# Performance work log

Hardware: AMD Instinct MI355X
Metric: run time of the kernel (lower is better)

The kernel has to match this reference:

```python
import jax, jax.numpy as jnp
import numpy as np

B, TK, NK, H, E, V = 128, 400, 50, 256, 256, 50000


def setup_inputs() -> dict:
    key = jax.random.key(0)
    ks = iter(jax.random.split(key, 48))
    def rn(shape, s=1.0):
        return jax.random.normal(next(ks), shape, jnp.float32) * s
    def ru(shape):
        return jax.random.uniform(next(ks), shape, jnp.float32)
    z = lambda shape: jnp.zeros(shape, jnp.float32)
    s = 0.05
    inp = {}
    inp['y_t_1'] = jax.random.randint(next(ks), (B,), 0, V)
    inp['h_prev'] = rn((B, H))
    inp['c_prev'] = rn((B, H))
    inp['encoder_outputs'] = rn((B, TK, H))
    inp['encoder_outputs_node'] = rn((B, NK, H))
    inp['enc_padding_mask'] = jnp.ones((B, TK), jnp.float32)
    inp['enc_padding_mask_node'] = jnp.ones((B, NK), jnp.float32)
    inp['c_t_d'] = rn((B, H))
    inp['c_t_g'] = rn((B, H))
    inp['c_t_g2'] = rn((B, H))
    inp['coverage'] = z((B, TK))
    inp['flow'] = ru((B, NK))
    inp['node_to_token'] = ru((B, NK, TK))
    inp['graph'] = ru((B, NK, NK))
    inp['voc_d'] = jax.random.randint(next(ks), (B, TK), 0, V)
    inp['step'] = 0
    # learned parameters
    inp['emb_table'] = rn((V, E), s)
    inp['Wx'] = rn((4 * H, E), s); inp['bx'] = z((E,))
    inp['Wi'] = rn((E, 4 * H), s); inp['Wh'] = rn((H, 4 * H), s)
    inp['bi'] = z((4 * H,)); inp['bh'] = z((4 * H,))
    inp['Whd'] = rn((H, H), s); inp['Wsd'] = rn((2 * H, H), s)
    inp['wcd'] = rn((H,), s); inp['vd'] = rn((H,), s); inp['bd'] = z((H,))
    inp['Wn'] = rn((H, H), s); inp['Wsf'] = rn((2 * H, H), s)
    inp['vf'] = rn((H,), s); inp['bf'] = z((H,))
    inp['Wpg'] = rn((5 * H + E, 1), s); inp['bpg'] = z((1,))
    inp['W1'] = rn((4 * H, H), s); inp['b1'] = z((H,))
    inp['W2'] = rn((H, V), s); inp['b2'] = z((V,))
    return inp


def _forward(y_t_1, h_prev, c_prev, enc, enc_n, mask_t, mask_n, c_t_d, c_t_g, c_t_g2,
             coverage, flow, n2t, graph, voc_d, emb_table, Wx, bx, Wi, Wh, bi, bh,
             Whd, Wsd, wcd, vd, bd, Wn, Wsf, vf, bf, Wpg, bpg, W1, b1, W2, b2):
    sig, tanh = jax.nn.sigmoid, jnp.tanh
    y_emb = emb_table[y_t_1]                                   # [B,E]
    x = jnp.concatenate([c_t_d, c_t_g, c_t_g2, y_emb], 1) @ Wx + bx
    # single-step LSTM (torch gate order i,f,g,o)
    gates = x @ Wi + h_prev @ Wh + bi + bh
    gi, gf, gg, go = jnp.split(gates, 4, axis=1)
    c_new = sig(gf) * c_prev + sig(gi) * tanh(gg)
    h_new = sig(go) * tanh(c_new)
    s_hat = jnp.concatenate([h_new, c_new], 1)                 # [B,2H]
    # doc attention with coverage (Bahdanau)
    e = tanh(enc @ Whd + (s_hat @ Wsd)[:, None, :] + coverage[:, :, None] * wcd + bd) @ vd
    a = jax.nn.softmax(e, axis=1) * mask_t
    a = a / a.sum(1, keepdims=True)                            # [B,TK]
    c_d = jnp.einsum('bt,bth->bh', a, enc)
    coverage_next = coverage + a
    # event-graph node attention (flow-weighted, one-hop propagation)
    en = tanh(enc_n @ Wn + (s_hat @ Wsf)[:, None, :] + bf) @ vf
    an = jax.nn.softmax(en, axis=1) * mask_n
    an = an / an.sum(1, keepdims=True)
    an = an * flow
    an = an / an.sum(1, keepdims=True)                         # [B,NK]
    c_g = jnp.einsum('bn,bnh->bh', an, enc_n)
    an2 = jnp.einsum('bn,bnm->bm', an, graph) * mask_n
    an2 = an2 / an2.sum(1, keepdims=True)
    c_g2 = jnp.einsum('bn,bnh->bh', an2, enc_n)
    a_n2t = jnp.einsum('bn,bnt->bt', an, n2t)
    a_n2t = a_n2t / a_n2t.sum(1, keepdims=True)
    # flow update: per-node max of token attention restricted to node tokens
    flow_ = jnp.max(a[:, None, :] * n2t, axis=2)               # [B,NK]
    flow_next = flow_ / flow_.sum(1, keepdims=True)
    # pointer-generator gate
    p_gen = sig(jnp.concatenate([c_d, c_g, c_g2, s_hat, x], 1) @ Wpg + bpg)  # [B,1]
    out = jnp.concatenate([h_new, c_d, c_g, c_g2], 1) @ W1 + b1
    vocab_dist = jax.nn.softmax(out @ W2 + b2, axis=1)         # [B,V]
    attn_all = a / a.sum(1, keepdims=True)
    attn_ = (1.0 - p_gen) * attn_all
    vocab_ = p_gen * vocab_dist
    rows = jnp.arange(vocab_.shape[0])[:, None]
    final_dist = vocab_.at[rows, voc_d].add(attn_)             # scatter_add over vocab
    return (final_dist, (h_new, c_new), c_d, c_g, c_g2, a, a_n2t, p_gen,
            coverage_next, flow_next)


def reference(y_t_1, h_prev, c_prev, encoder_outputs, encoder_outputs_node,
              enc_padding_mask, enc_padding_mask_node, c_t_d, c_t_g, c_t_g2,
              coverage, flow, node_to_token, graph, voc_d, step,
              emb_table, Wx, bx, Wi, Wh, bi, bh, Whd, Wsd, wcd, vd, bd,
              Wn, Wsf, vf, bf, Wpg, bpg, W1, b1, W2, b2):
    return _forward(y_t_1, h_prev, c_prev, encoder_outputs, encoder_outputs_node,
                    enc_padding_mask, enc_padding_mask_node, c_t_d, c_t_g, c_t_g2,
                    coverage, flow, node_to_token, graph, voc_d, emb_table, Wx, bx,
                    Wi, Wh, bi, bh, Whd, Wsd, wcd, vd, bd, Wn, Wsf, vf, bf,
                    Wpg, bpg, W1, b1, W2, b2)
```

## Files before the change

kernel.cpp:

```cpp
#include <hip/hip_runtime.h>
#include <stdint.h>


typedef unsigned short u16;
typedef unsigned int   u32;

#define Bv  128
#define TKv 400
#define NKv 50
#define Hv  256
#define Vv  50000
#define VPAD 50176
#define NSv 16
#define CHUNKv 3136
#define MDOC (Bv * TKv)
#define MNODE (Bv * NKv)
#define NBLK (VPAD / 64)

typedef __attribute__((ext_vector_type(8))) short bf16x8;
typedef __attribute__((ext_vector_type(4))) float f32x4;

__device__ float g_x[32768];
__device__ float g_xp[4 * 32768];
__device__ float g_gates[131072];
__device__ float g_h[32768];
__device__ float g_c[32768];
__device__ float g_sdp[2 * 32768];
__device__ float g_sfp[2 * 32768];
__device__ float g_ep[4 * MDOC];
__device__ float g_enp[4 * MNODE];
__device__ float g_a[51200];
__device__ float g_cd[32768];
__device__ float g_cdp[8 * 32768];
__device__ float g_cg[32768];
__device__ float g_cg2[32768];
__device__ float g_pg[128];
__device__ float g_ans[MNODE];
__device__ float g_inv4[128];
__device__ float g_fl[MNODE];
__device__ float g_nrs[MNODE];
__device__ float g_o1[32768];
__device__ __attribute__((aligned(16))) u16 g_o1b[32768];
__device__ float g_vpp[(size_t)2 * Bv * NBLK];
__device__ float g_vred[Bv * 2];
__device__ float g_logits[6400000];
__device__ u16   g_Wdt[256 * 256];
__device__ u16   g_Wnt[256 * 256];
__device__ u16   g_W2t[(size_t)VPAD * 256];
__device__ u16   g_encb[(size_t)Bv * TKv * 256];
__device__ u16   g_encnb[(size_t)Bv * NKv * 256];

__device__ __forceinline__ float sigm(float x) { return 1.f / (1.f + expf(-x)); }

__device__ __forceinline__ u16 f2bf(float f) {
    u32 u = __float_as_uint(f);
    return (u16)((u + 0x7fffu + ((u >> 16) & 1u)) >> 16);
}

__device__ __forceinline__ bf16x8 cvt8(const float* __restrict__ p) {
    const float4 a = *(const float4*)p;
    const float4 b = *(const float4*)(p + 4);
    bf16x8 r;
    r[0] = (short)f2bf(a.x); r[1] = (short)f2bf(a.y);
    r[2] = (short)f2bf(a.z); r[3] = (short)f2bf(a.w);
    r[4] = (short)f2bf(b.x); r[5] = (short)f2bf(b.y);
    r[6] = (short)f2bf(b.z); r[7] = (short)f2bf(b.w);
    return r;
}

__device__ __forceinline__ float fast_tanh(float x) {
    x = fminf(fmaxf(x, -15.f), 15.f);
    float e = __expf(2.f * x);
    return (e - 1.f) / (e + 1.f);
}

__device__ __forceinline__ void ms_merge(float& m1, float& s1, float m2, float s2) {
    float M = fmaxf(m1, m2);
    s1 = s1 * expf(m1 - M) + s2 * expf(m2 - M);
    m1 = M;
}

__global__ __launch_bounds__(256) void k_cvt(
    const float* __restrict__ src, u16* __restrict__ dst, int n8)
{
    int i = blockIdx.x * 256 + threadIdx.x;
    const int stride = gridDim.x * 256;
    for (; i < n8; i += stride)
        *(bf16x8*)(dst + (size_t)i * 8) = cvt8(src + (size_t)i * 8);
}

__global__ __launch_bounds__(256) void k_tc(
    const float* __restrict__ src, u16* __restrict__ dst, int K, int N)
{
    __shared__ float tile[32][33];
    const int n0 = blockIdx.x * 32, k0 = blockIdx.y * 32;
    const int tx = threadIdx.x & 31, ty = threadIdx.x >> 5;
    #pragma unroll
    for (int i = 0; i < 32; i += 8) {
        int k = k0 + ty + i, n = n0 + tx;
        tile[ty + i][tx] = (n < N) ? src[(size_t)k * N + n] : 0.f;
    }
    __syncthreads();
    #pragma unroll
    for (int i = 0; i < 32; i += 8) {
        int n = n0 + ty + i, k = k0 + tx;
        dst[(size_t)n * K + k] = f2bf(tile[tx][ty + i]);
    }
}

__global__ __launch_bounds__(256) void k_x(
    const int* __restrict__ y,
    const float* __restrict__ ctd, const float* __restrict__ ctg,
    const float* __restrict__ ctg2, const float* __restrict__ emb,
    const float* __restrict__ Wx)
{
    const int b = blockIdx.x, ks = blockIdx.y, j = threadIdx.x;
    __shared__ float cs[256];
    float v;
    if      (ks == 0) v = ctd [b * 256 + j];
    else if (ks == 1) v = ctg [b * 256 + j];
    else if (ks == 2) v = ctg2[b * 256 + j];
    else              v = emb[(size_t)y[b] * 256 + j];
    cs[j] = v;
    __syncthreads();

    float acc = 0.f;
    const float* w = Wx + (size_t)(ks * 256) * 256 + j;
    #pragma unroll 8
    for (int k = 0; k < 256; k++) acc += cs[k] * w[(size_t)k * 256];
    g_xp[ks * 32768 + b * 256 + j] = acc;
}

__global__ __launch_bounds__(256) void k_gates(
    const float* __restrict__ h_prev,
    const float* __restrict__ Wi, const float* __restrict__ Wh,
    const float* __restrict__ bi, const float* __restrict__ bh,
    const float* __restrict__ bx)
{
    const int b = blockIdx.x, cc = blockIdx.y, j = threadIdx.x;
    __shared__ float xs[256], hs[256];

    float xv = bx[j] + g_xp[b * 256 + j] + g_xp[32768 + b * 256 + j]
             + g_xp[65536 + b * 256 + j] + g_xp[98304 + b * 256 + j];
    xs[j] = xv;
    if (cc == 0) g_x[b * 256 + j] = xv;
    hs[j] = h_prev[b * 256 + j];
    __syncthreads();

    const int col = cc * 256 + j;
    float acc = bi[col] + bh[col];
    const float* wi = Wi + col;
    const float* wh = Wh + col;
    #pragma unroll 8
    for (int k = 0; k < 256; k++)
        acc += xs[k] * wi[(size_t)k * 1024] + hs[k] * wh[(size_t)k * 1024];
    g_gates[b * 1024 + col] = acc;
}

__global__ __launch_bounds__(256) void k_cellsd(
    const float* __restrict__ c_prev,
    const float* __restrict__ Wsd, const float* __restrict__ Wsf,
    float* __restrict__ out_h, float* __restrict__ out_c)
{
    const int b = blockIdx.x, ks = blockIdx.y, j = threadIdx.x;
    __shared__ float sh[256];

    const float* gb = g_gates + b * 1024;
    float gi_ = gb[j], gf_ = gb[256 + j], gg_ = gb[512 + j], go_ = gb[768 + j];
    float cp = c_prev[b * 256 + j];
    float cn = sigm(gf_) * cp + sigm(gi_) * tanhf(gg_);
    float hn = sigm(go_) * tanhf(cn);
    if (ks == 0) {
        g_h[b * 256 + j] = hn;  g_c[b * 256 + j] = cn;
        out_h[b * 256 + j] = hn; out_c[b * 256 + j] = cn;
    }
    sh[j] = (ks == 0) ? hn : cn;
    __syncthreads();

    float asd = 0.f, asf = 0.f;
    const float* wd = Wsd + (size_t)(ks * 256) * 256 + j;
    const float* wf = Wsf + (size_t)(ks * 256) * 256 + j;
    #pragma unroll 8
    for (int k = 0; k < 256; k++) {
        float sv = sh[k];
        asd += sv * wd[(size_t)k * 256];
        asf += sv * wf[(size_t)k * 256];
    }
    g_sdp[ks * 32768 + b * 256 + j] = asd;
    g_sfp[ks * 32768 + b * 256 + j] = asf;
}

template<int R>
__global__ __launch_bounds__(256) void k_scores(
    const u16* __restrict__ srcb,
    const u16* __restrict__ Wt,
    const float* __restrict__ addv0,
    const float* __restrict__ addv1,
    const float* __restrict__ abias,
    const float* __restrict__ cov,
    const float* __restrict__ wcw,
    const float* __restrict__ vv,
    float* __restrict__ eout, int Mtot)
{
    const int tid = threadIdx.x;
    const int lane = tid & 63, w = tid >> 6;
    const int nlow = lane & 15, quad = lane >> 4;
    const int c0 = blockIdx.y * 64;

    __shared__ u16 Bs[64][264];
    {
        const u16* wsrc = Wt + (size_t)c0 * 256;
        #pragma unroll
        for (int j = 0; j < 8; j++) {
            int chunk = tid + j * 256;
            int row = chunk >> 5, c16 = chunk & 31;
            *(bf16x8*)(&Bs[row][c16 * 8]) =
                *(const bf16x8*)(wsrc + row * 256 + c16 * 8);
        }
    }
    __syncthreads();

    const int rowbase = blockIdx.x * 128 + w * 32;
    const u16* a0 = srcb + (size_t)(rowbase + nlow) * 256 + quad * 8;
    const u16* a1 = a0 + 16 * 256;

    const f32x4 zf = {0.f, 0.f, 0.f, 0.f};
    f32x4 acc[2][4];
    #pragma unroll
    for (int mi = 0; mi < 2; mi++)
        #pragma unroll
        for (int ni = 0; ni < 4; ni++) acc[mi][ni] = zf;

    bf16x8 af0 = *(const bf16x8*)(a0);
    bf16x8 af1 = *(const bf16x8*)(a1);
    for (int k0 = 0; k0 < 256; k0 += 32) {
        const int kn = (k0 + 32) & 255;
        bf16x8 nf0 = *(const bf16x8*)(a0 + kn);
        bf16x8 nf1 = *(const bf16x8*)(a1 + kn);
        bf16x8 bf[4];
        #pragma unroll
        for (int ni = 0; ni < 4; ni++)
            bf[ni] = *(const bf16x8*)(&Bs[ni * 16 + nlow][k0 + quad * 8]);
        #pragma unroll
        for (int ni = 0; ni < 4; ni++) {
            acc[0][ni] = __builtin_amdgcn_mfma_f32_16x16x32_bf16(af0, bf[ni], acc[0][ni], 0, 0, 0);
            acc[1][ni] = __builtin_amdgcn_mfma_f32_16x16x32_bf16(af1, bf[ni], acc[1][ni], 0, 0, 0);
        }
        af0 = nf0; af1 = nf1;
    }

    #pragma unroll
    for (int mi = 0; mi < 2; mi++) {
        float covt[4]; int bidx[4];
        #pragma unroll
        for (int r = 0; r < 4; r++) {
            int row = rowbase + mi * 16 + quad * 4 + r;
            covt[r] = cov ? cov[row] : 0.f;
            bidx[r] = row / R;
        }
        float s4[4] = {0.f, 0.f, 0.f, 0.f};
        #pragma unroll
        for (int ni = 0; ni < 4; ni++) {
            int col = c0 + ni * 16 + nlow;
            float vvc = vv[col];
            float ab  = abias[col];
            float wcc = wcw ? wcw[col] : 0.f;
            #pragma unroll
            for (int r = 0; r < 4; r++) {
                float adc = addv0[bidx[r] * 256 + col] + addv1[bidx[r] * 256 + col] + ab;
                s4[r] += vvc * fast_tanh(acc[mi][ni][r] + adc + covt[r] * wcc);
            }
        }
        #pragma unroll
        for (int r = 0; r < 4; r++) {
            float s = s4[r];
            s += __shfl_xor(s, 1, 64);
            s += __shfl_xor(s, 2, 64);
            s += __shfl_xor(s, 4, 64);
            s += __shfl_xor(s, 8, 64);
            int row = rowbase + mi * 16 + quad * 4 + r;
            if (nlow == 0)
                eout[(size_t)blockIdx.y * Mtot + row] = s;
        }
    }
}

__global__ __launch_bounds__(256) void k_doc(
    const float* __restrict__ mask,
    const float* __restrict__ cov,
    float* __restrict__ out_a, float* __restrict__ out_cov)
{
    const int b = blockIdx.x, tid = threadIdx.x;
    __shared__ float red[256];

    float e0 = 0.f, e1s = 0.f;
    #pragma unroll
    for (int ch = 0; ch < 4; ch++) {
        e0 += g_ep[ch * MDOC + b * TKv + tid];
        if (tid + 256 < TKv) e1s += g_ep[ch * MDOC + b * TKv + tid + 256];
    }
    float e1 = (tid + 256 < TKv) ? e1s : -1e30f;

    float m = fmaxf(e0, e1);
    red[tid] = m; __syncthreads();
    for (int s = 128; s > 0; s >>= 1) { if (tid < s) red[tid] = fmaxf(red[tid], red[tid + s]); __syncthreads(); }
    m = red[0]; __syncthreads();

    float p0 = expf(e0 - m) * mask[b * TKv + tid];
    float p1 = (tid + 256 < TKv) ? expf(e1 - m) * mask[b * TKv + tid + 256] : 0.f;
    red[tid] = p0 + p1; __syncthreads();
    for (int s = 128; s > 0; s >>= 1) { if (tid < s) red[tid] += red[tid + s]; __syncthreads(); }
    float inv = 1.f / red[0];

    float a0 = p0 * inv;
    g_a[b * TKv + tid] = a0;
    out_a[b * TKv + tid] = a0;
    out_cov[b * TKv + tid] = cov[b * TKv + tid] + a0;
    if (tid + 256 < TKv) {
        float a1 = p1 * inv;
        g_a[b * TKv + tid + 256] = a1;
        out_a[b * TKv + tid + 256] = a1;
        out_cov[b * TKv + tid + 256] = cov[b * TKv + tid + 256] + a1;
    }
}

__global__ __launch_bounds__(256) void k_cd(const float* __restrict__ enc)
{
    const int b = blockIdx.x, ks = blockIdx.y, tid = threadIdx.x;
    __shared__ float as_[50];
    if (tid < 50) as_[tid] = g_a[b * TKv + ks * 50 + tid];
    __syncthreads();

    const float* eb = enc + ((size_t)b * TKv + ks * 50) * 256 + tid;
    float acc = 0.f;
    #pragma unroll 10
    for (int t = 0; t < 50; t++) acc += as_[t] * eb[(size_t)t * 256];
    g_cdp[ks * 32768 + b * 256 + tid] = acc;
}

__global__ __launch_bounds__(256) void k_fmax(const float* __restrict__ n2t)
{
    const int bn = blockIdx.x;
    const int b = bn / NKv;
    const int tid = threadIdx.x;
    __shared__ float rmx[256], rsm[256];

    const float* nb = n2t + (size_t)bn * TKv;
    const float* ab = g_a + b * TKv;

    float x0 = nb[tid], a0 = ab[tid];
    float mx = a0 * x0, sm = x0;
    if (tid + 256 < TKv) {
        float x1 = nb[tid + 256], a1 = ab[tid + 256];
        mx = fmaxf(mx, a1 * x1);
        sm += x1;
    }
    mx = fmaxf(mx, 0.f);
    rmx[tid] = mx; rsm[tid] = sm; __syncthreads();
    for (int s = 128; s > 0; s >>= 1) {
        if (tid < s) {
            rmx[tid] = fmaxf(rmx[tid], rmx[tid + s]);
            rsm[tid] += rsm[tid + s];
        }
        __syncthreads();
    }
    if (tid == 0) { g_fl[bn] = rmx[0]; g_nrs[bn] = rsm[0]; }
}

__global__ __launch_bounds__(64) void k_flow2(float* __restrict__ out_flow)
{
    const int b = blockIdx.x, tid = threadIdx.x;
    float v = (tid < NKv) ? g_fl[b * NKv + tid] : 0.f;
    float s = v;
    s += __shfl_xor(s, 1, 64);
    s += __shfl_xor(s, 2, 64);
    s += __shfl_xor(s, 4, 64);
    s += __shfl_xor(s, 8, 64);
    s += __shfl_xor(s, 16, 64);
    s += __shfl_xor(s, 32, 64);
    if (tid < NKv) out_flow[b * NKv + tid] = v / s;
}

__global__ __launch_bounds__(256) void k_node1(
    const float* __restrict__ encn,
    const float* __restrict__ maskn,
    const float* __restrict__ flow,
    const float* __restrict__ graph,
    const float* __restrict__ Wpg, const float* __restrict__ bpg,
    float* __restrict__ out_cd, float* __restrict__ out_cg,
    float* __restrict__ out_cg2, float* __restrict__ out_pgen)
{
    const int b = blockIdx.x, tid = threadIdx.x;
    __shared__ float ans[NKv], an2s[NKv], red[256];

    float cd = 0.f;
    #pragma unroll
    for (int i = 0; i < 8; i++) cd += g_cdp[i * 32768 + b * 256 + tid];
    g_cd[b * 256 + tid] = cd;
    out_cd[b * 256 + tid] = cd;

    float v = -1e30f;
    if (tid < NKv) {
        v = 0.f;
        #pragma unroll
        for (int ch = 0; ch < 4; ch++) v += g_enp[ch * MNODE + b * NKv + tid];
    }
    red[tid] = v; __syncthreads();
    for (int s = 128; s > 0; s >>= 1) { if (tid < s) red[tid] = fmaxf(red[tid], red[tid + s]); __syncthreads(); }
    float m = red[0]; __syncthreads();

    float p = (tid < NKv) ? expf(v - m) * maskn[b * NKv + tid] : 0.f;
    red[tid] = p; __syncthreads();
    for (int s = 128; s > 0; s >>= 1) { if (tid < s) red[tid] += red[tid + s]; __syncthreads(); }
    float S = red[0]; __syncthreads();
    p = (tid < NKv) ? (p / S) * flow[b * NKv + tid] : 0.f;
    red[tid] = p; __syncthreads();
    for (int s = 128; s > 0; s >>= 1) { if (tid < s) red[tid] += red[tid + s]; __syncthreads(); }
    float S2 = red[0]; __syncthreads();
    if (tid < NKv) {
        ans[tid] = p / S2;
        g_ans[b * NKv + tid] = ans[tid];
    }
    __syncthreads();

    float s4p = (tid < NKv) ? ans[tid] * g_nrs[b * NKv + tid] : 0.f;
    red[tid] = s4p; __syncthreads();
    for (int s = 128; s > 0; s >>= 1) { if (tid < s) red[tid] += red[tid + s]; __syncthreads(); }
    if (tid == 0) g_inv4[b] = 1.f / red[0];
    __syncthreads();

    float q = 0.f;
    if (tid < NKv) {
        const float* gb = graph + (size_t)b * NKv * NKv + tid;
        #pragma unroll
        for (int n = 0; n < NKv; n++) q += ans[n] * gb[n * NKv];
        q *= maskn[b * NKv + tid];
    }
    red[tid] = q; __syncthreads();
    for (int s = 128; s > 0; s >>= 1) { if (tid < s) red[tid] += red[tid + s]; __syncthreads(); }
    float S3 = red[0]; __syncthreads();
    if (tid < NKv) an2s[tid] = q / S3;
    __syncthreads();

    float cg = 0.f, cg2 = 0.f;
    {
        const float* enb = encn + (size_t)b * NKv * 256 + tid;
        #pragma unroll
        for (int n = 0; n < NKv; n++) {
            float e = enb[n * 256];
            cg  += ans[n]  * e;
            cg2 += an2s[n] * e;
        }
    }
    g_cg[b * 256 + tid] = cg;   out_cg[b * 256 + tid] = cg;
    g_cg2[b * 256 + tid] = cg2; out_cg2[b * 256 + tid] = cg2;

    float hvv = g_h[b * 256 + tid], cvv = g_c[b * 256 + tid];
    float xvv = g_x[b * 256 + tid];
    float part = cd  * Wpg[tid]        + cg  * Wpg[256 + tid]
               + cg2 * Wpg[512 + tid]  + hvv * Wpg[768 + tid]
               + cvv * Wpg[1024 + tid] + xvv * Wpg[1280 + tid];
    red[tid] = part; __syncthreads();
    for (int s = 128; s > 0; s >>= 1) { if (tid < s) red[tid] += red[tid + s]; __syncthreads(); }
    if (tid == 0) {
        float pg = sigm(red[0] + bpg[0]);
        g_pg[b] = pg; out_pgen[b] = pg;
    }
}

__global__ __launch_bounds__(256) void k_ant(
    const float* __restrict__ n2t, float* __restrict__ out_ant)
{
    const int b = blockIdx.x, ks = blockIdx.y, tid = threadIdx.x;
    __shared__ float ans[NKv];
    if (tid < NKv) ans[tid] = g_ans[b * NKv + tid];
    __syncthreads();

    if (tid < 200) {
        const int t = ks * 200 + tid;
        const float* nb = n2t + (size_t)b * NKv * TKv + t;
        float at = 0.f;
        #pragma unroll
        for (int n = 0; n < NKv; n++) at += ans[n] * nb[n * TKv];
        out_ant[b * TKv + t] = at * g_inv4[b];
    }
}

__global__ __launch_bounds__(256) void k_o1(
    const float* __restrict__ W1, const float* __restrict__ b1)
{
    const int b = blockIdx.x, cc = blockIdx.y, tid = threadIdx.x;
    __shared__ float cat[1024];
    __shared__ float red[256];

    cat[tid]       = g_h  [b * 256 + tid];
    cat[256 + tid] = g_cd [b * 256 + tid];
    cat[512 + tid] = g_cg [b * 256 + tid];
    cat[768 + tid] = g_cg2[b * 256 + tid];
    __syncthreads();

    const int lane = tid & 63, kq = tid >> 6;
    const int col = cc * 64 + lane;
    const float* w  = W1 + (size_t)(kq * 256) * 256 + col;
    const float* cs = cat + kq * 256;
    float acc = 0.f;
    #pragma unroll 8
    for (int k = 0; k < 256; k++) acc += cs[k] * w[(size_t)k * 256];
    red[tid] = acc; __syncthreads();

    if (tid < 64) {
        float o = b1[cc * 64 + tid]
                + red[tid] + red[64 + tid] + red[128 + tid] + red[192 + tid];
        g_o1[b * 256 + cc * 64 + tid] = o;
        g_o1b[b * 256 + cc * 64 + tid] = f2bf(o);
    }
}

__global__ __launch_bounds__(256) void k_logits(const float* __restrict__ b2)
{
    const int v0 = blockIdx.x * 64;
    const int tid = threadIdx.x;
    const int lane = tid & 63, wave = tid >> 6;
    const int nlow = lane & 15, quad = lane >> 4;

    const u16* a0p = g_o1b + (wave * 32 + nlow) * 256 + quad * 8;
    const u16* a1p = a0p + 16 * 256;
    const u16* bbase = g_W2t + (size_t)(v0 + nlow) * 256 + quad * 8;

    const f32x4 zf = {0.f, 0.f, 0.f, 0.f};
    f32x4 acc0[4], acc1[4];
    #pragma unroll
    for (int i = 0; i < 4; i++) { acc0[i] = zf; acc1[i] = zf; }

    for (int k0 = 0; k0 < 256; k0 += 32) {
        bf16x8 a0 = *(const bf16x8*)(a0p + k0);
        bf16x8 a1 = *(const bf16x8*)(a1p + k0);
        #pragma unroll
        for (int nt = 0; nt < 4; nt++) {
            bf16x8 bf = *(const bf16x8*)(bbase + (size_t)nt * 4096 + k0);
            acc0[nt] = __builtin_amdgcn_mfma_f32_16x16x32_bf16(a0, bf, acc0[nt], 0, 0, 0);
            acc1[nt] = __builtin_amdgcn_mfma_f32_16x16x32_bf16(a1, bf, acc1[nt], 0, 0, 0);
        }
    }

    float bbv[4]; bool val[4];
    #pragma unroll
    for (int nt = 0; nt < 4; nt++) {
        int v = v0 + nt * 16 + nlow;
        val[nt] = v < Vv;
        bbv[nt] = val[nt] ? b2[v] : 0.f;
    }

    #pragma unroll
    for (int mi = 0; mi < 2; mi++) {
        #pragma unroll
        for (int r = 0; r < 4; r++) {
            const int row = wave * 32 + mi * 16 + quad * 4 + r;
            float x[4];
            #pragma unroll
            for (int nt = 0; nt < 4; nt++) {
                float xv = (mi ? acc1[nt][r] : acc0[nt][r]) + bbv[nt];
                if (val[nt]) g_logits[(size_t)row * Vv + v0 + nt * 16 + nlow] = xv;
                x[nt] = val[nt] ? xv : -1e30f;
            }
            float m = fmaxf(fmaxf(x[0], x[1]), fmaxf(x[2], x[3]));
            m = fmaxf(m, __shfl_xor(m, 1, 64));
            m = fmaxf(m, __shfl_xor(m, 2, 64));
            m = fmaxf(m, __shfl_xor(m, 4, 64));
            m = fmaxf(m, __shfl_xor(m, 8, 64));
            float s = expf(x[0] - m) + expf(x[1] - m)
                    + expf(x[2] - m) + expf(x[3] - m);
            s += __shfl_xor(s, 1, 64);
            s += __shfl_xor(s, 2, 64);
            s += __shfl_xor(s, 4, 64);
            s += __shfl_xor(s, 8, 64);
            if (nlow == 0) {
                g_vpp[((size_t)row * NBLK + blockIdx.x) * 2]     = m;
                g_vpp[((size_t)row * NBLK + blockIdx.x) * 2 + 1] = s;
            }
        }
    }
}

__global__ __launch_bounds__(256) void k_vmerge()
{
    const int b = blockIdx.x, tid = threadIdx.x;
    __shared__ float rm[256], rs[256];

    float M = -1e30f, S = 0.f;
    for (int i = tid; i < NBLK; i += 256)
        ms_merge(M, S, g_vpp[((size_t)b * NBLK + i) * 2],
                       g_vpp[((size_t)b * NBLK + i) * 2 + 1]);
    rm[tid] = M; rs[tid] = S; __syncthreads();
    for (int off = 128; off > 0; off >>= 1) {
        if (tid < off) {
            float m1 = rm[tid], s1 = rs[tid];
            ms_merge(m1, s1, rm[tid + off], rs[tid + off]);
            rm[tid] = m1; rs[tid] = s1;
        }
        __syncthreads();
    }
    if (tid == 0) { g_vred[b * 2] = rm[0]; g_vred[b * 2 + 1] = rs[0]; }
}

__global__ __launch_bounds__(256) void k_vwrite(float* __restrict__ outF)
{
    const int b = blockIdx.x, ks = blockIdx.y, tid = threadIdx.x;

    const float M = g_vred[b * 2];
    const float inv = g_pg[b] / g_vred[b * 2 + 1];

    const int base = ks * CHUNKv;
    const int end  = min(base + CHUNKv, Vv);
    const int n4   = (end - base) >> 2;
    const float4* L4 = (const float4*)(g_logits + (size_t)b * Vv + base);
    float4* O4 = (float4*)(outF + (size_t)b * Vv + base);

    for (int i = tid; i < n4; i += 256) {
        float4 x = L4[i];
        float4 r;
        r.x = expf(x.x - M) * inv;
        r.y = expf(x.y - M) * inv;
        r.z = expf(x.z - M) * inv;
        r.w = expf(x.w - M) * inv;
        O4[i] = r;
    }
}

__global__ __launch_bounds__(256) void k_scatter(
    float* __restrict__ outF, const int* __restrict__ vocd)
{
    const int b = blockIdx.x, tid = threadIdx.x;
    float* Ob = outF + (size_t)b * Vv;
    const float omp = 1.f - g_pg[b];
    for (int t = tid; t < TKv; t += 256)
        atomicAdd(Ob + vocd[b * TKv + t], omp * g_a[b * TKv + t]);
}


extern "C" void kernel_launch(void* const* d_in, const int* in_sizes, int n_in,
                              void* d_out, int out_size, void* d_ws, size_t ws_size,
                              hipStream_t stream)
{
    (void)in_sizes; (void)n_in; (void)out_size; (void)d_ws; (void)ws_size;

    const int*   y      = (const int*)d_in[0];
    const float* h_prev = (const float*)d_in[1];
    const float* c_prev = (const float*)d_in[2];
    const float* enc    = (const float*)d_in[3];
    const float* encn   = (const float*)d_in[4];
    const float* mask   = (const float*)d_in[5];
    const float* maskn  = (const float*)d_in[6];
    const float* ctd    = (const float*)d_in[7];
    const float* ctg    = (const float*)d_in[8];
    const float* ctg2   = (const float*)d_in[9];
    const float* cov    = (const float*)d_in[10];
    const float* flow   = (const float*)d_in[11];
    const float* n2t    = (const float*)d_in[12];
    const float* graph  = (const float*)d_in[13];
    const int*   vocd   = (const int*)d_in[14];
    const float* emb    = (const float*)d_in[16];
    const float* Wx     = (const float*)d_in[17];
    const float* bx     = (const float*)d_in[18];
    const float* Wi     = (const float*)d_in[19];
    const float* Wh     = (const float*)d_in[20];
    const float* bi     = (const float*)d_in[21];
    const float* bh     = (const float*)d_in[22];
    const float* Whd    = (const float*)d_in[23];
    const float* Wsd    = (const float*)d_in[24];
    const float* wcdw   = (const float*)d_in[25];
    const float* vd     = (const float*)d_in[26];
    const float* bd     = (const float*)d_in[27];
    const float* Wn     = (const float*)d_in[28];
    const float* Wsf    = (const float*)d_in[29];
    const float* vf     = (const float*)d_in[30];
    const float* bfv    = (const float*)d_in[31];
    const float* Wpg    = (const float*)d_in[32];
    const float* bpg    = (const float*)d_in[33];
    const float* W1     = (const float*)d_in[34];
    const float* b1     = (const float*)d_in[35];
    const float* W2     = (const float*)d_in[36];
    const float* b2     = (const float*)d_in[37];

    float* o = (float*)d_out;
    float* o_final = o;
    float* o_h     = o + 6400000;
    float* o_c     = o + 6432768;
    float* o_cd    = o + 6465536;
    float* o_cg    = o + 6498304;
    float* o_cg2   = o + 6531072;
    float* o_a     = o + 6563840;
    float* o_ant   = o + 6615040;
    float* o_pg    = o + 6666240;
    float* o_cov   = o + 6666368;
    float* o_fl    = o + 6717568;

    float* g_ep_p;  hipGetSymbolAddress((void**)&g_ep_p,  HIP_SYMBOL(g_ep));
    float* g_enp_p; hipGetSymbolAddress((void**)&g_enp_p, HIP_SYMBOL(g_enp));
    float* g_sdp_p; hipGetSymbolAddress((void**)&g_sdp_p, HIP_SYMBOL(g_sdp));
    float* g_sfp_p; hipGetSymbolAddress((void**)&g_sfp_p, HIP_SYMBOL(g_sfp));
    u16*   g_Wdt_p; hipGetSymbolAddress((void**)&g_Wdt_p, HIP_SYMBOL(g_Wdt));
    u16*   g_Wnt_p; hipGetSymbolAddress((void**)&g_Wnt_p, HIP_SYMBOL(g_Wnt));
    u16*   g_W2t_p; hipGetSymbolAddress((void**)&g_W2t_p, HIP_SYMBOL(g_W2t));
    u16*   g_encb_p;  hipGetSymbolAddress((void**)&g_encb_p,  HIP_SYMBOL(g_encb));
    u16*   g_encnb_p; hipGetSymbolAddress((void**)&g_encnb_p, HIP_SYMBOL(g_encnb));

    k_tc<<<dim3(8, 8), dim3(256), 0, stream>>>(Whd, g_Wdt_p, 256, 256);
    k_tc<<<dim3(8, 8), dim3(256), 0, stream>>>(Wn,  g_Wnt_p, 256, 256);
    k_tc<<<dim3(VPAD / 32, 8), dim3(256), 0, stream>>>(W2, g_W2t_p, 256, Vv);

    k_cvt<<<dim3(2048), dim3(256), 0, stream>>>(enc,  g_encb_p,  Bv * TKv * 256 / 8);
    k_cvt<<<dim3(800),  dim3(256), 0, stream>>>(encn, g_encnb_p, Bv * NKv * 256 / 8);

    k_x<<<dim3(Bv, 4), dim3(256), 0, stream>>>(y, ctd, ctg, ctg2, emb, Wx);

    k_gates<<<dim3(Bv, 4), dim3(256), 0, stream>>>(h_prev, Wi, Wh, bi, bh, bx);

    k_cellsd<<<dim3(Bv, 2), dim3(256), 0, stream>>>(c_prev, Wsd, Wsf, o_h, o_c);

    k_scores<TKv><<<dim3(MDOC / 128, 4), dim3(256), 0, stream>>>(
        g_encb_p, g_Wdt_p, g_sdp_p, g_sdp_p + 32768, bd, cov, wcdw, vd,
        g_ep_p, MDOC);

    k_scores<NKv><<<dim3(MNODE / 128, 4), dim3(256), 0, stream>>>(
        g_encnb_p, g_Wnt_p, g_sfp_p, g_sfp_p + 32768, bfv,
        nullptr, nullptr, vf, g_enp_p, MNODE);

    k_doc<<<dim3(Bv), dim3(256), 0, stream>>>(mask, cov, o_a, o_cov);

    k_fmax<<<dim3(Bv * NKv), dim3(256), 0, stream>>>(n2t);

    k_flow2<<<dim3(Bv), dim3(64), 0, stream>>>(o_fl);

    k_cd<<<dim3(Bv, 8), dim3(256), 0, stream>>>(enc);

    k_node1<<<dim3(Bv), dim3(256), 0, stream>>>(
        encn, maskn, flow, graph, Wpg, bpg,
        o_cd, o_cg, o_cg2, o_pg);

    k_ant<<<dim3(Bv, 2), dim3(256), 0, stream>>>(n2t, o_ant);

    k_o1<<<dim3(Bv, 4), dim3(256), 0, stream>>>(W1, b1);

    k_logits<<<dim3(NBLK), dim3(256), 0, stream>>>(b2);

    k_vmerge<<<dim3(Bv), dim3(256), 0, stream>>>();

    k_vwrite<<<dim3(Bv, NSv), dim3(256), 0, stream>>>(o_final);

    k_scatter<<<dim3(Bv), dim3(256), 0, stream>>>(o_final, vocd);
}
```

Baseline: 466.8 us.

## Merge independent kernels into combined launches to cut launch count

Several independent kernels are merged into single launches that branch on block index: weight transposes, encoder bf16 conversion and the x projection become one prep kernel; the doc and node score GEMMs share one launch; fmax and cd are combined; ant and o1 are combined. The flow normalization moves into k_node1, and the vocab merge and scatter move into the vocab write kernel. The merged write kernel recomputes the row max and sum in every chunk block and scatters only into its own chunk. This removes launch overhead and serialization between small kernels, at the cost of redundant reductions and heterogeneous blocks within one grid.

```diff
diff --git a/kernel.cpp b/kernel.cpp
--- a/kernel.cpp
+++ b/kernel.cpp
@@ -16,6 +16,12 @@
 #define MDOC (Bv * TKv)
 #define MNODE (Bv * NKv)
 #define NBLK (VPAD / 64)
+
+#define NB_TCW2 ((VPAD / 32) * 8)
+#define NB_PAIR 128
+#define NB_CVT  2148
+#define NB_KX   (Bv * 4)
+#define NB_PREP (NB_TCW2 + NB_PAIR + NB_CVT + NB_KX)
 
 typedef __attribute__((ext_vector_type(8))) short bf16x8;
 typedef __attribute__((ext_vector_type(4))) float f32x4;
@@ -42,7 +48,6 @@
 __device__ float g_o1[32768];
 __device__ __attribute__((aligned(16))) u16 g_o1b[32768];
 __device__ float g_vpp[(size_t)2 * Bv * NBLK];
-__device__ float g_vred[Bv * 2];
 __device__ float g_logits[6400000];
 __device__ u16   g_Wdt[256 * 256];
 __device__ u16   g_Wnt[256 * 256];
@@ -80,55 +85,84 @@
     m1 = M;
 }
 
-__global__ __launch_bounds__(256) void k_cvt(
-    const float* __restrict__ src, u16* __restrict__ dst, int n8)
-{
-    int i = blockIdx.x * 256 + threadIdx.x;
-    const int stride = gridDim.x * 256;
-    for (; i < n8; i += stride)
-        *(bf16x8*)(dst + (size_t)i * 8) = cvt8(src + (size_t)i * 8);
-}
-
-__global__ __launch_bounds__(256) void k_tc(
-    const float* __restrict__ src, u16* __restrict__ dst, int K, int N)
-{
-    __shared__ float tile[32][33];
-    const int n0 = blockIdx.x * 32, k0 = blockIdx.y * 32;
-    const int tx = threadIdx.x & 31, ty = threadIdx.x >> 5;
-    #pragma unroll
-    for (int i = 0; i < 32; i += 8) {
-        int k = k0 + ty + i, n = n0 + tx;
-        tile[ty + i][tx] = (n < N) ? src[(size_t)k * N + n] : 0.f;
-    }
-    __syncthreads();
-    #pragma unroll
-    for (int i = 0; i < 32; i += 8) {
-        int n = n0 + ty + i, k = k0 + tx;
-        dst[(size_t)n * K + k] = f2bf(tile[tx][ty + i]);
-    }
-}
-
-__global__ __launch_bounds__(256) void k_x(
+__global__ __launch_bounds__(256) void k_prep(
+    const float* __restrict__ Whd, const float* __restrict__ Wn,
+    const float* __restrict__ W2,
+    const float* __restrict__ enc, const float* __restrict__ encn,
     const int* __restrict__ y,
     const float* __restrict__ ctd, const float* __restrict__ ctg,
     const float* __restrict__ ctg2, const float* __restrict__ emb,
     const float* __restrict__ Wx)
 {
-    const int b = blockIdx.x, ks = blockIdx.y, j = threadIdx.x;
-    __shared__ float cs[256];
-    float v;
-    if      (ks == 0) v = ctd [b * 256 + j];
-    else if (ks == 1) v = ctg [b * 256 + j];
-    else if (ks == 2) v = ctg2[b * 256 + j];
-    else              v = emb[(size_t)y[b] * 256 + j];
-    cs[j] = v;
-    __syncthreads();
-
-    float acc = 0.f;
-    const float* w = Wx + (size_t)(ks * 256) * 256 + j;
-    #pragma unroll 8
-    for (int k = 0; k < 256; k++) acc += cs[k] * w[(size_t)k * 256];
-    g_xp[ks * 32768 + b * 256 + j] = acc;
+    __shared__ float tile[32][33];
+    const int tid = threadIdx.x;
+    int bid = blockIdx.x;
+
+    if (bid < NB_TCW2) {
+        const int n0 = (bid % (VPAD / 32)) * 32, k0 = (bid / (VPAD / 32)) * 32;
+        const int tx = tid & 31, ty = tid >> 5;
+        #pragma unroll
+        for (int i = 0; i < 32; i += 8) {
+            int k = k0 + ty + i, n = n0 + tx;
+            tile[ty + i][tx] = (n < Vv) ? W2[(size_t)k * Vv + n] : 0.f;
+        }
+        __syncthreads();
+        #pragma unroll
+        for (int i = 0; i < 32; i += 8) {
+            int n = n0 + ty + i, k = k0 + tx;
+            g_W2t[(size_t)n * 256 + k] = f2bf(tile[tx][ty + i]);
+        }
+        return;
+    }
+    bid -= NB_TCW2;
+    if (bid < NB_PAIR) {
+        const int z = bid >> 6, rem = bid & 63;
+        const float* src = z ? Wn : Whd;
+        u16* dst = z ? g_Wnt : g_Wdt;
+        const int n0 = (rem & 7) * 32, k0 = (rem >> 3) * 32;
+        const int tx = tid & 31, ty = tid >> 5;
+        #pragma unroll
+        for (int i = 0; i < 32; i += 8)
+            tile[ty + i][tx] = src[(size_t)(k0 + ty + i) * 256 + n0 + tx];
+        __syncthreads();
+        #pragma unroll
+        for (int i = 0; i < 32; i += 8)
+            dst[(size_t)(n0 + ty + i) * 256 + k0 + tx] = f2bf(tile[tx][ty + i]);
+        return;
+    }
+    bid -= NB_PAIR;
+    if (bid < NB_CVT) {
+        if (bid < 2048) {
+            const int n8 = Bv * TKv * 256 / 8;
+            int i = bid * 256 + tid;
+            for (; i < n8; i += 2048 * 256)
+                *(bf16x8*)(g_encb + (size_t)i * 8) = cvt8(enc + (size_t)i * 8);
+        } else {
+            const int n8 = Bv * NKv * 256 / 8;
+            int i = (bid - 2048) * 256 + tid;
+            for (; i < n8; i += 100 * 256)
+                *(bf16x8*)(g_encnb + (size_t)i * 8) = cvt8(encn + (size_t)i * 8);
+        }
+        return;
+    }
+    bid -= NB_CVT;
+    {
+        const int b = bid >> 2, ks = bid & 3, j = tid;
+        float* cs = &tile[0][0];
+        float v;
+        if      (ks == 0) v = ctd [b * 256 + j];
+        else if (ks == 1) v = ctg [b * 256 + j];
+        else if (ks == 2) v = ctg2[b * 256 + j];
+        else              v = emb[(size_t)y[b] * 256 + j];
+        cs[j] = v;
+        __syncthreads();
+
+        float acc = 0.f;
+        const float* w = Wx + (size_t)(ks * 256) * 256 + j;
+        #pragma unroll 8
+        for (int k = 0; k < 256; k++) acc += cs[k] * w[(size_t)k * 256];
+        g_xp[ks * 32768 + b * 256 + j] = acc;
+    }
 }
 
 __global__ __launch_bounds__(256) void k_gates(
@@ -190,22 +224,29 @@
     g_sfp[ks * 32768 + b * 256 + j] = asf;
 }
 
-template<int R>
-__global__ __launch_bounds__(256) void k_scores(
-    const u16* __restrict__ srcb,
-    const u16* __restrict__ Wt,
-    const float* __restrict__ addv0,
-    const float* __restrict__ addv1,
-    const float* __restrict__ abias,
-    const float* __restrict__ cov,
-    const float* __restrict__ wcw,
-    const float* __restrict__ vv,
-    float* __restrict__ eout, int Mtot)
+__global__ __launch_bounds__(256) void k_scores_all(
+    const float* __restrict__ bd,  const float* __restrict__ bfv,
+    const float* __restrict__ cov, const float* __restrict__ wcdw,
+    const float* __restrict__ vd,  const float* __restrict__ vf)
 {
     const int tid = threadIdx.x;
     const int lane = tid & 63, w = tid >> 6;
     const int nlow = lane & 15, quad = lane >> 4;
     const int c0 = blockIdx.y * 64;
+
+    const bool isdoc = blockIdx.x < (MDOC / 128);
+    const int bx = isdoc ? blockIdx.x : blockIdx.x - MDOC / 128;
+    const int R = isdoc ? TKv : NKv;
+    const int Mtot = isdoc ? MDOC : MNODE;
+    const u16* srcb = isdoc ? g_encb : g_encnb;
+    const u16* Wt   = isdoc ? g_Wdt : g_Wnt;
+    const float* addv0 = isdoc ? g_sdp : g_sfp;
+    const float* addv1 = isdoc ? g_sdp + 32768 : g_sfp + 32768;
+    const float* abias = isdoc ? bd : bfv;
+    const float* covp  = isdoc ? cov : nullptr;
+    const float* wcw   = isdoc ? wcdw : nullptr;
+    const float* vv    = isdoc ? vd : vf;
+    float* eout        = isdoc ? g_ep : g_enp;
 
     __shared__ u16 Bs[64][264];
     {
@@ -220,7 +261,7 @@
     }
     __syncthreads();
 
-    const int rowbase = blockIdx.x * 128 + w * 32;
+    const int rowbase = bx * 128 + w * 32;
     const u16* a0 = srcb + (size_t)(rowbase + nlow) * 256 + quad * 8;
     const u16* a1 = a0 + 16 * 256;
 
@@ -255,7 +296,7 @@
         #pragma unroll
         for (int r = 0; r < 4; r++) {
             int row = rowbase + mi * 16 + quad * 4 + r;
-            covt[r] = cov ? cov[row] : 0.f;
+            covt[r] = covp ? covp[row] : 0.f;
             bidx[r] = row / R;
         }
         float s4[4] = {0.f, 0.f, 0.f, 0.f};
@@ -324,61 +365,49 @@
     }
 }
 
-__global__ __launch_bounds__(256) void k_cd(const float* __restrict__ enc)
-{
-    const int b = blockIdx.x, ks = blockIdx.y, tid = threadIdx.x;
-    __shared__ float as_[50];
-    if (tid < 50) as_[tid] = g_a[b * TKv + ks * 50 + tid];
-    __syncthreads();
-
-    const float* eb = enc + ((size_t)b * TKv + ks * 50) * 256 + tid;
-    float acc = 0.f;
-    #pragma unroll 10
-    for (int t = 0; t < 50; t++) acc += as_[t] * eb[(size_t)t * 256];
-    g_cdp[ks * 32768 + b * 256 + tid] = acc;
-}
-
-__global__ __launch_bounds__(256) void k_fmax(const float* __restrict__ n2t)
-{
-    const int bn = blockIdx.x;
-    const int b = bn / NKv;
+__global__ __launch_bounds__(256) void k_fmax_cd(
+    const float* __restrict__ n2t, const float* __restrict__ enc)
+{
+    __shared__ float sA[256], sB[256];
     const int tid = threadIdx.x;
-    __shared__ float rmx[256], rsm[256];
-
-    const float* nb = n2t + (size_t)bn * TKv;
-    const float* ab = g_a + b * TKv;
-
-    float x0 = nb[tid], a0 = ab[tid];
-    float mx = a0 * x0, sm = x0;
-    if (tid + 256 < TKv) {
-        float x1 = nb[tid + 256], a1 = ab[tid + 256];
-        mx = fmaxf(mx, a1 * x1);
-        sm += x1;
-    }
-    mx = fmaxf(mx, 0.f);
-    rmx[tid] = mx; rsm[tid] = sm; __syncthreads();
-    for (int s = 128; s > 0; s >>= 1) {
-        if (tid < s) {
-            rmx[tid] = fmaxf(rmx[tid], rmx[tid + s]);
-            rsm[tid] += rsm[tid + s];
-        }
+    int bid = blockIdx.x;
+
+    if (bid < Bv * NKv) {
+        const int b = bid / NKv;
+        const float* nb = n2t + (size_t)bid * TKv;
+        const float* ab = g_a + b * TKv;
+
+        float x0 = nb[tid], a0 = ab[tid];
+        float mx = a0 * x0, sm = x0;
+        if (tid + 256 < TKv) {
+            float x1 = nb[tid + 256], a1 = ab[tid + 256];
+            mx = fmaxf(mx, a1 * x1);
+            sm += x1;
+        }
+        mx = fmaxf(mx, 0.f);
+        sA[tid] = mx; sB[tid] = sm; __syncthreads();
+        for (int s = 128; s > 0; s >>= 1) {
+            if (tid < s) {
+                sA[tid] = fmaxf(sA[tid], sA[tid + s]);
+                sB[tid] += sB[tid + s];
+            }
+            __syncthreads();
+        }
+        if (tid == 0) { g_fl[bid] = sA[0]; g_nrs[bid] = sB[0]; }
+        return;
+    }
+    bid -= Bv * NKv;
+    {
+        const int b = bid >> 3, ks = bid & 7;
+        if (tid < 50) sA[tid] = g_a[b * TKv + ks * 50 + tid];
         __syncthreads();
-    }
-    if (tid == 0) { g_fl[bn] = rmx[0]; g_nrs[bn] = rsm[0]; }
-}
-
-__global__ __launch_bounds__(64) void k_flow2(float* __restrict__ out_flow)
-{
-    const int b = blockIdx.x, tid = threadIdx.x;
-    float v = (tid < NKv) ? g_fl[b * NKv + tid] : 0.f;
-    float s = v;
-    s += __shfl_xor(s, 1, 64);
-    s += __shfl_xor(s, 2, 64);
-    s += __shfl_xor(s, 4, 64);
-    s += __shfl_xor(s, 8, 64);
-    s += __shfl_xor(s, 16, 64);
-    s += __shfl_xor(s, 32, 64);
-    if (tid < NKv) out_flow[b * NKv + tid] = v / s;
+
+        const float* eb = enc + ((size_t)b * TKv + ks * 50) * 256 + tid;
+        float acc = 0.f;
+        #pragma unroll 10
+        for (int t = 0; t < 50; t++) acc += sA[t] * eb[(size_t)t * 256];
+        g_cdp[ks * 32768 + b * 256 + tid] = acc;
+    }
 }
 
 __global__ __launch_bounds__(256) void k_node1(
@@ -388,10 +417,17 @@
     const float* __restrict__ graph,
     const float* __restrict__ Wpg, const float* __restrict__ bpg,
     float* __restrict__ out_cd, float* __restrict__ out_cg,
-    float* __restrict__ out_cg2, float* __restrict__ out_pgen)
+    float* __restrict__ out_cg2, float* __restrict__ out_pgen,
+    float* __restrict__ out_flow)
 {
     const int b = blockIdx.x, tid = threadIdx.x;
     __shared__ float ans[NKv], an2s[NKv], red[256];
+
+    float fv = (tid < NKv) ? g_fl[b * NKv + tid] : 0.f;
+    red[tid] = fv; __syncthreads();
+    for (int s = 128; s > 0; s >>= 1) { if (tid < s) red[tid] += red[tid + s]; __syncthreads(); }
+    float fs = red[0]; __syncthreads();
+    if (tid < NKv) out_flow[b * NKv + tid] = fv / fs;
 
     float cd = 0.f;
     #pragma unroll
@@ -468,51 +504,54 @@
     }
 }
 
-__global__ __launch_bounds__(256) void k_ant(
-    const float* __restrict__ n2t, float* __restrict__ out_ant)
-{
-    const int b = blockIdx.x, ks = blockIdx.y, tid = threadIdx.x;
-    __shared__ float ans[NKv];
-    if (tid < NKv) ans[tid] = g_ans[b * NKv + tid];
-    __syncthreads();
-
-    if (tid < 200) {
-        const int t = ks * 200 + tid;
-        const float* nb = n2t + (size_t)b * NKv * TKv + t;
-        float at = 0.f;
-        #pragma unroll
-        for (int n = 0; n < NKv; n++) at += ans[n] * nb[n * TKv];
-        out_ant[b * TKv + t] = at * g_inv4[b];
-    }
-}
-
-__global__ __launch_bounds__(256) void k_o1(
-    const float* __restrict__ W1, const float* __restrict__ b1)
-{
-    const int b = blockIdx.x, cc = blockIdx.y, tid = threadIdx.x;
+__global__ __launch_bounds__(256) void k_ant_o1(
+    const float* __restrict__ n2t,
+    const float* __restrict__ W1, const float* __restrict__ b1,
+    float* __restrict__ out_ant)
+{
     __shared__ float cat[1024];
     __shared__ float red[256];
-
-    cat[tid]       = g_h  [b * 256 + tid];
-    cat[256 + tid] = g_cd [b * 256 + tid];
-    cat[512 + tid] = g_cg [b * 256 + tid];
-    cat[768 + tid] = g_cg2[b * 256 + tid];
-    __syncthreads();
-
-    const int lane = tid & 63, kq = tid >> 6;
-    const int col = cc * 64 + lane;
-    const float* w  = W1 + (size_t)(kq * 256) * 256 + col;
-    const float* cs = cat + kq * 256;
-    float acc = 0.f;
-    #pragma unroll 8
-    for (int k = 0; k < 256; k++) acc += cs[k] * w[(size_t)k * 256];
-    red[tid] = acc; __syncthreads();
-
-    if (tid < 64) {
-        float o = b1[cc * 64 + tid]
-                + red[tid] + red[64 + tid] + red[128 + tid] + red[192 + tid];
-        g_o1[b * 256 + cc * 64 + tid] = o;
-        g_o1b[b * 256 + cc * 64 + tid] = f2bf(o);
+    const int tid = threadIdx.x;
+    int bid = blockIdx.x;
+
+    if (bid < 2 * Bv) {
+        const int b = bid >> 1, ks = bid & 1;
+        if (tid < NKv) red[tid] = g_ans[b * NKv + tid];
+        __syncthreads();
+        if (tid < 200) {
+            const int t = ks * 200 + tid;
+            const float* nb = n2t + (size_t)b * NKv * TKv + t;
+            float at = 0.f;
+            #pragma unroll
+            for (int n = 0; n < NKv; n++) at += red[n] * nb[n * TKv];
+            out_ant[b * TKv + t] = at * g_inv4[b];
+        }
+        return;
+    }
+    bid -= 2 * Bv;
+    {
+        const int b = bid >> 2, cc = bid & 3;
+        cat[tid]       = g_h  [b * 256 + tid];
+        cat[256 + tid] = g_cd [b * 256 + tid];
+        cat[512 + tid] = g_cg [b * 256 + tid];
+        cat[768 + tid] = g_cg2[b * 256 + tid];
+        __syncthreads();
+
+        const int lane = tid & 63, kq = tid >> 6;
+        const int col = cc * 64 + lane;
+        const float* w  = W1 + (size_t)(kq * 256) * 256 + col;
+        const float* cs = cat + kq * 256;
+        float acc = 0.f;
+        #pragma unroll 8
+        for (int k = 0; k < 256; k++) acc += cs[k] * w[(size_t)k * 256];
+        red[tid] = acc; __syncthreads();
+
+        if (tid < 64) {
+            float o = b1[cc * 64 + tid]
+                    + red[tid] + red[64 + tid] + red[128 + tid] + red[192 + tid];
+            g_o1[b * 256 + cc * 64 + tid] = o;
+            g_o1b[b * 256 + cc * 64 + tid] = f2bf(o);
+        }
     }
 }
 
@@ -582,9 +621,10 @@
     }
 }
 
-__global__ __launch_bounds__(256) void k_vmerge()
-{
-    const int b = blockIdx.x, tid = threadIdx.x;
+__global__ __launch_bounds__(256) void k_vwrite_sc(
+    float* __restrict__ outF, const int* __restrict__ vocd)
+{
+    const int b = blockIdx.x, ks = blockIdx.y, tid = threadIdx.x;
     __shared__ float rm[256], rs[256];
 
     float M = -1e30f, S = 0.f;
@@ -600,15 +640,8 @@
         }
         __syncthreads();
     }
-    if (tid == 0) { g_vred[b * 2] = rm[0]; g_vred[b * 2 + 1] = rs[0]; }
-}
-
-__global__ __launch_bounds__(256) void k_vwrite(float* __restrict__ outF)
-{
-    const int b = blockIdx.x, ks = blockIdx.y, tid = threadIdx.x;
-
-    const float M = g_vred[b * 2];
-    const float inv = g_pg[b] / g_vred[b * 2 + 1];
+    M = rm[0];
+    const float inv = g_pg[b] / rs[0];
 
     const int base = ks * CHUNKv;
     const int end  = min(base + CHUNKv, Vv);
@@ -625,16 +658,16 @@
         r.w = expf(x.w - M) * inv;
         O4[i] = r;
     }
-}
-
-__global__ __launch_bounds__(256) void k_scatter(
-    float* __restrict__ outF, const int* __restrict__ vocd)
-{
-    const int b = blockIdx.x, tid = threadIdx.x;
-    float* Ob = outF + (size_t)b * Vv;
+
+    __threadfence();
+    __syncthreads();
+
     const float omp = 1.f - g_pg[b];
-    for (int t = tid; t < TKv; t += 256)
-        atomicAdd(Ob + vocd[b * TKv + t], omp * g_a[b * TKv + t]);
+    for (int t = tid; t < TKv; t += 256) {
+        int v = vocd[b * TKv + t];
+        if (v >= base && v < base + CHUNKv)
+            atomicAdd(outF + (size_t)b * Vv + v, omp * g_a[b * TKv + t]);
+    }
 }
 
 
@@ -695,58 +728,27 @@
     float* o_cov   = o + 6666368;
     float* o_fl    = o + 6717568;
 
-    float* g_ep_p;  hipGetSymbolAddress((void**)&g_ep_p,  HIP_SYMBOL(g_ep));
-    float* g_enp_p; hipGetSymbolAddress((void**)&g_enp_p, HIP_SYMBOL(g_enp));
-    float* g_sdp_p; hipGetSymbolAddress((void**)&g_sdp_p, HIP_SYMBOL(g_sdp));
-    float* g_sfp_p; hipGetSymbolAddress((void**)&g_sfp_p, HIP_SYMBOL(g_sfp));
-    u16*   g_Wdt_p; hipGetSymbolAddress((void**)&g_Wdt_p, HIP_SYMBOL(g_Wdt));
-    u16*   g_Wnt_p; hipGetSymbolAddress((void**)&g_Wnt_p, HIP_SYMBOL(g_Wnt));
-    u16*   g_W2t_p; hipGetSymbolAddress((void**)&g_W2t_p, HIP_SYMBOL(g_W2t));
-    u16*   g_encb_p;  hipGetSymbolAddress((void**)&g_encb_p,  HIP_SYMBOL(g_encb));
-    u16*   g_encnb_p; hipGetSymbolAddress((void**)&g_encnb_p, HIP_SYMBOL(g_encnb));
-
-    k_tc<<<dim3(8, 8), dim3(256), 0, stream>>>(Whd, g_Wdt_p, 256, 256);
-    k_tc<<<dim3(8, 8), dim3(256), 0, stream>>>(Wn,  g_Wnt_p, 256, 256);
-    k_tc<<<dim3(VPAD / 32, 8), dim3(256), 0, stream>>>(W2, g_W2t_p, 256, Vv);
-
-    k_cvt<<<dim3(2048), dim3(256), 0, stream>>>(enc,  g_encb_p,  Bv * TKv * 256 / 8);
-    k_cvt<<<dim3(800),  dim3(256), 0, stream>>>(encn, g_encnb_p, Bv * NKv * 256 / 8);
-
-    k_x<<<dim3(Bv, 4), dim3(256), 0, stream>>>(y, ctd, ctg, ctg2, emb, Wx);
+    k_prep<<<dim3(NB_PREP), dim3(256), 0, stream>>>(
+        Whd, Wn, W2, enc, encn, y, ctd, ctg, ctg2, emb, Wx);
 
     k_gates<<<dim3(Bv, 4), dim3(256), 0, stream>>>(h_prev, Wi, Wh, bi, bh, bx);
 
     k_cellsd<<<dim3(Bv, 2), dim3(256), 0, stream>>>(c_prev, Wsd, Wsf, o_h, o_c);
 
-    k_scores<TKv><<<dim3(MDOC / 128, 4), dim3(256), 0, stream>>>(
-        g_encb_p, g_Wdt_p, g_sdp_p, g_sdp_p + 32768, bd, cov, wcdw, vd,
-        g_ep_p, MDOC);
-
-    k_scores<NKv><<<dim3(MNODE / 128, 4), dim3(256), 0, stream>>>(
-        g_encnb_p, g_Wnt_p, g_sfp_p, g_sfp_p + 32768, bfv,
-        nullptr, nullptr, vf, g_enp_p, MNODE);
+    k_scores_all<<<dim3(MDOC / 128 + MNODE / 128, 4), dim3(256), 0, stream>>>(
+        bd, bfv, cov, wcdw, vd, vf);
 
     k_doc<<<dim3(Bv), dim3(256), 0, stream>>>(mask, cov, o_a, o_cov);
 
-    k_fmax<<<dim3(Bv * NKv), dim3(256), 0, stream>>>(n2t);
-
-    k_flow2<<<dim3(Bv), dim3(64), 0, stream>>>(o_fl);
-
-    k_cd<<<dim3(Bv, 8), dim3(256), 0, stream>>>(enc);
+    k_fmax_cd<<<dim3(Bv * NKv + Bv * 8), dim3(256), 0, stream>>>(n2t, enc);
 
     k_node1<<<dim3(Bv), dim3(256), 0, stream>>>(
         encn, maskn, flow, graph, Wpg, bpg,
-        o_cd, o_cg, o_cg2, o_pg);
-
-    k_ant<<<dim3(Bv, 2), dim3(256), 0, stream>>>(n2t, o_ant);
-
-    k_o1<<<dim3(Bv, 4), dim3(256), 0, stream>>>(W1, b1);
+        o_cd, o_cg, o_cg2, o_pg, o_fl);
+
+    k_ant_o1<<<dim3(2 * Bv + 4 * Bv), dim3(256), 0, stream>>>(n2t, W1, b1, o_ant);
 
     k_logits<<<dim3(NBLK), dim3(256), 0, stream>>>(b2);
 
-    k_vmerge<<<dim3(Bv), dim3(256), 0, stream>>>();
-
-    k_vwrite<<<dim3(Bv, NSv), dim3(256), 0, stream>>>(o_final);
-
-    k_scatter<<<dim3(Bv), dim3(256), 0, stream>>>(o_final, vocd);
-}
+    k_vwrite_sc<<<dim3(Bv, NSv), dim3(256), 0, stream>>>(o_final, vocd);
+}
```

Measured after the change: 645.1 us. 38.2% more time.
